# Optimization experiments

Hardware: AMD Instinct MI355X
Metric: run time of the kernel (lower is better)

The kernel has to match this reference:

```python
import jax, jax.numpy as jnp
import numpy as np

WINDOW, HOP = 20, 10   # SplitSignal_cplx(2, window_size=20, hop_length=10)
EPS = 1e-6             # eigenvalue clip for matrix log
RIDGE = 1e-3           # SPD ridge to keep matrices positive definite


def sparsemax(z):
    # Closed-form sparsemax projection onto the simplex (Martins & Astudillo 2016),
    # mirroring use_sparsemax_as_convex_layer (QP projection onto the simplex).
    zs = jnp.sort(z)[::-1]
    k = jnp.arange(1, z.shape[0] + 1, dtype=z.dtype)
    zc = jnp.cumsum(zs)
    support = 1.0 + k * zs > zc
    kz_i = jnp.sum(support).astype(jnp.int32)
    kz = kz_i.astype(z.dtype)
    tau = (zc[kz_i - 1] - 1.0) / kz
    return jnp.maximum(z - tau, 0.0)


def _sym(S):
    return 0.5 * (S + jnp.swapaxes(S, -1, -2))


def logm(S):
    # batched symmetric matrix log via eigh (LogEig / barycenter log-map)
    w, V = jnp.linalg.eigh(_sym(S))
    lw = jnp.log(jnp.maximum(w, EPS))
    return jnp.einsum('...ij,...j,...kj->...ik', V, lw, V)


def expm(S):
    w, V = jnp.linalg.eigh(_sym(S))
    return jnp.einsum('...ij,...j,...kj->...ik', V, jnp.exp(w), V)


def frame_signal(x):
    # x: [B, 2, T] -> frames [B, 2*n_win, WINDOW]  (SplitSignal)
    B, Cc, T = x.shape
    n_win = (T - WINDOW) // HOP + 1
    idx = jnp.arange(n_win)[:, None] * HOP + jnp.arange(WINDOW)[None, :]
    f = x[:, :, idx]                      # [B, 2, n_win, WINDOW]
    return f.reshape(B, Cc * n_win, WINDOW)


def covpool(f):
    # covariance pooling over frames -> SPD [B, WINDOW, WINDOW]
    N = f.shape[1]
    f = f - f.mean(axis=1, keepdims=True)
    cov = jnp.einsum('bnd,bne->bde', f, f) / (N - 1)
    return cov + RIDGE * jnp.eye(WINDOW, dtype=f.dtype)


def cell(S, W, alpha):
    # One DARTS-style SPD cell: candidate BiMap ops + per-channel weighted
    # Riemannian (log-Euclidean) barycenter  G = expm(sum_k w_k logm(op_k(S))).
    # S: [B, C, d, d];  W: [2, K, d, do] (2 branches -> channel doubling);
    # alpha: [K] architecture logits.
    w = sparsemax(alpha)                               # [K]
    cand = jnp.einsum('mkji,bcjl,mkln->mkbcin', W, S, W)  # [2, K, B, C, do, do]
    do = cand.shape[-1]
    cand = cand + RIDGE * jnp.eye(do, dtype=S.dtype)
    L = logm(cand)                                     # log-map of every candidate
    G = expm(jnp.einsum('k,mkbcij->mbcij', w, L))      # weighted barycenter [2,B,C,do,do]
    B = S.shape[0]
    return jnp.moveaxis(G, 0, 1).reshape(B, -1, do, do)  # channels double: [B, 2C, do, do]


def reference(x, W_stem, W_op0, W_op1, W_op2, alphas, W_cls, b_cls):
    f = frame_signal(x)                                # [B, 798, 20]
    cov = covpool(f)                                   # [B, 20, 20]
    # stem BiMap: W^T S W
    S = jnp.einsum('ji,bjk,kl->bil', W_stem, cov, W_stem)[:, None]  # [B,1,20,20]
    S = S + RIDGE * jnp.eye(WINDOW, dtype=x.dtype)
    S = cell(S, W_op0, alphas[0])                      # [B, 2, 10, 10] (reduce 20->10)
    S = cell(S, W_op1, alphas[1])                      # [B, 4, 10, 10]
    S = cell(S, W_op2, alphas[2])                      # [B, 8, 10, 10]
    out = logm(S).reshape(S.shape[0], -1)              # LogEig + flatten -> [B, 800]
    return out @ W_cls + b_cls


def setup_inputs() -> dict:
    key = jax.random.key(0)
    ks = jax.random.split(key, 8)
    B, T = 2048, 4000
    d_in, d_out, K, n_cls = 20, 10, 6, 10
    x = jax.random.normal(ks[0], (B, 2, T), jnp.float32)
    W_stem = jax.random.normal(ks[1], (d_in, d_in), jnp.float32) / np.sqrt(d_in)
    W_op0 = jax.random.normal(ks[2], (2, K, d_in, d_out), jnp.float32) / np.sqrt(d_in)
    W_op1 = jax.random.normal(ks[3], (2, K, d_out, d_out), jnp.float32) / np.sqrt(d_out)
    W_op2 = jax.random.normal(ks[4], (2, K, d_out, d_out), jnp.float32) / np.sqrt(d_out)
    alphas = 0.001 * jax.random.normal(ks[5], (3, K), jnp.float32)
    W_cls = jax.random.normal(ks[6], (8 * d_out * d_out, n_cls), jnp.float32) * 0.02
    b_cls = jnp.zeros((n_cls,), jnp.float32)
    return dict(x=x, W_stem=W_stem, W_op0=W_op0, W_op1=W_op1, W_op2=W_op2,
                alphas=alphas, W_cls=W_cls, b_cls=b_cls)
```

## Files before the change

kernel.cpp:

```cpp
#include <hip/hip_runtime.h>
#include <math.h>

#define WIN   20
#define NWIN  399
#define NCH   2
#define TLEN  4000
#define NFR   798
#define KOPS  6
#define NB    2048
#define EPSV  1e-6f
#define RIDGE 1e-3f

#define TIX(i,j) ((i)*10 - (i)*((i)+1)/2 + (j))

__device__ __forceinline__ float frcp(float x){float r;asm("v_rcp_f32 %0, %1":"=v"(r):"v"(x));return r;}
__device__ __forceinline__ float frsq(float x){float r;asm("v_rsq_f32 %0, %1":"=v"(r):"v"(x));return r;}
__device__ __forceinline__ float fsqr(float x){float r;asm("v_sqrt_f32 %0, %1":"=v"(r):"v"(x));return r;}

__device__ __forceinline__ void jacobi10(float* A, float* V) {
#pragma unroll
  for (int i = 0; i < 100; i++) V[i] = 0.f;
#pragma unroll
  for (int i = 0; i < 10; i++) V[i * 11] = 1.f;

  for (int sweep = 0; sweep < 7; ++sweep) {
    float off = 0.f, dia = 0.f;
#pragma unroll
    for (int p = 0; p < 10; p++) {
      float d = A[TIX(p, p)];
      dia = fmaf(d, d, dia);
#pragma unroll
      for (int q = p + 1; q < 10; q++) { float o = A[TIX(p, q)]; off = fmaf(o, o, off); }
    }
    float fro2 = dia + 2.f * off;
    if (__ballot(off > 1e-11f * fro2) == 0ull) break;
    float skipthr = 1e-12f * fro2;

#pragma unroll
    for (int p = 0; p < 10; p++) {
#pragma unroll
      for (int q = p + 1; q < 10; q++) {
        float apq = A[TIX(p, q)];
        if (__ballot(apq * apq > skipthr) == 0ull) continue;
        float app = A[TIX(p, p)];
        float aqq = A[TIX(q, q)];
        bool rot = fabsf(apq) > 1e-30f;
        float theta = (aqq - app) * frcp(rot ? 2.f * apq : 1.f);
        float t = copysignf(frcp(fabsf(theta) + fsqr(fmaf(theta, theta, 1.f))), theta);
        t = rot ? t : 0.f;
        float c = frsq(fmaf(t, t, 1.f));
        float s = t * c;
#pragma unroll
        for (int j = 0; j < 10; j++) {
          if (j == p || j == q) continue;
          const int jp = (j < p) ? TIX(j, p) : TIX(p, j);
          const int jq = (j < q) ? TIX(j, q) : TIX(q, j);
          float ajp = A[jp], ajq = A[jq];
          A[jp] = fmaf(c, ajp, -s * ajq);
          A[jq] = fmaf(s, ajp, c * ajq);
        }
        A[TIX(p, p)] = fmaf(-t, apq, A[TIX(p, p)]);
        A[TIX(q, q)] = fmaf(t, apq, A[TIX(q, q)]);
        A[TIX(p, q)] = 0.0f;
#pragma unroll
        for (int i = 0; i < 10; i++) {
          float vip = V[i * 10 + p], viq = V[i * 10 + q];
          V[i * 10 + p] = fmaf(c, vip, -s * viq);
          V[i * 10 + q] = fmaf(s, vip, c * viq);
        }
      }
    }
  }
}

__global__ __launch_bounds__(256) void k_cov_stem(const float* __restrict__ x,
                                                  const float* __restrict__ Wst,
                                                  float* __restrict__ Sout) {
  __shared__ float xl[NCH * TLEN];
  __shared__ float pT[2][NCH][100];
  __shared__ float pQ[2][NCH][100];
  __shared__ float bsum[NCH][10];
  __shared__ float b0v[NCH][10];
  __shared__ float b399v[NCH][10];
  __shared__ float cov[400];
  __shared__ float wst[400];
  __shared__ float tmp[400];
  int b = blockIdx.x, tid = threadIdx.x;
  const float4* xg = (const float4*)(x + (size_t)b * NCH * TLEN);
  float4* xl4 = (float4*)xl;
  for (int i = tid; i < NCH * TLEN / 4; i += 256) xl4[i] = xg[i];
  for (int i = tid; i < 400; i += 256) wst[i] = Wst[i];
  __syncthreads();

  if (tid < 200) {
    int grp = tid / 100;
    int c = (tid % 100) / 50;
    int r = tid % 50;
    int seg = r / 25, tile = r % 25;
    int d0 = (tile / 5) * 2, e0 = (tile % 5) * 2;
    const float* xc = xl + c * TLEN;
    int i0 = seg * 200;
    int i1 = grp ? ((seg == 1) ? 399 : 200) : (i0 + 200);
    int eoff = grp ? 10 : 0;
    float a00 = 0.f, a01 = 0.f, a10 = 0.f, a11 = 0.f;
    for (int i = i0; i < i1; i++) {
      float2 bd = *(const float2*)(xc + i * 10 + d0);
      float2 be = *(const float2*)(xc + i * 10 + eoff + e0);
      a00 = fmaf(bd.x, be.x, a00); a01 = fmaf(bd.x, be.y, a01);
      a10 = fmaf(bd.y, be.x, a10); a11 = fmaf(bd.y, be.y, a11);
    }
    float* dst = grp ? &pQ[seg][c][0] : &pT[seg][c][0];
    dst[d0 * 10 + e0] = a00;
    dst[d0 * 10 + e0 + 1] = a01;
    dst[(d0 + 1) * 10 + e0] = a10;
    dst[(d0 + 1) * 10 + e0 + 1] = a11;
  } else if (tid >= 200 && tid < 220) {
    int c = (tid - 200) / 10, d = (tid - 200) % 10;
    const float* xc = xl + c * TLEN;
    float s = 0.f;
    for (int i = 0; i < 400; i++) s += xc[i * 10 + d];
    bsum[c][d] = s;
    b0v[c][d] = xc[d];
    b399v[c][d] = xc[3990 + d];
  }
  __syncthreads();

  const float invN = 1.0f / (float)NFR;
  const float invN1 = 1.0f / (float)(NFR - 1);
  for (int o = tid; o < 400; o += 256) {
    int d = o / 20, e = o % 20;
    int dl = d % 10, el = e % 10;
    float s2;
    if (d < 10 && e < 10)
      s2 = (pT[0][0][dl * 10 + el] + pT[1][0][dl * 10 + el] - b399v[0][dl] * b399v[0][el]) +
           (pT[0][1][dl * 10 + el] + pT[1][1][dl * 10 + el] - b399v[1][dl] * b399v[1][el]);
    else if (d >= 10 && e >= 10)
      s2 = (pT[0][0][dl * 10 + el] + pT[1][0][dl * 10 + el] - b0v[0][dl] * b0v[0][el]) +
           (pT[0][1][dl * 10 + el] + pT[1][1][dl * 10 + el] - b0v[1][dl] * b0v[1][el]);
    else if (d < 10)
      s2 = pQ[0][0][dl * 10 + el] + pQ[1][0][dl * 10 + el] +
           pQ[0][1][dl * 10 + el] + pQ[1][1][dl * 10 + el];
    else
      s2 = pQ[0][0][el * 10 + dl] + pQ[1][0][el * 10 + dl] +
           pQ[0][1][el * 10 + dl] + pQ[1][1][el * 10 + dl];
    float md = (d < 10) ? (bsum[0][dl] - b399v[0][dl] + bsum[1][dl] - b399v[1][dl])
                        : (bsum[0][dl] - b0v[0][dl] + bsum[1][dl] - b0v[1][dl]);
    float me = (e < 10) ? (bsum[0][el] - b399v[0][el] + bsum[1][el] - b399v[1][el])
                        : (bsum[0][el] - b0v[0][el] + bsum[1][el] - b0v[1][el]);
    float v = (s2 - (float)NFR * (md * invN) * (me * invN)) * invN1;
    if (d == e) v += RIDGE;
    cov[o] = v;
  }
  __syncthreads();
  for (int o = tid; o < 400; o += 256) {
    int j = o / 20, l = o % 20;
    float acc = 0.f;
    for (int k2 = 0; k2 < 20; k2++) acc = fmaf(cov[j * 20 + k2], wst[k2 * 20 + l], acc);
    tmp[o] = acc;
  }
  __syncthreads();
  for (int o = tid; o < 400; o += 256) {
    int i = o / 20, l = o % 20;
    float acc = 0.f;
    for (int j = 0; j < 20; j++) acc = fmaf(wst[j * 20 + i], tmp[j * 20 + l], acc);
    if (i == l) acc += RIDGE;
    Sout[b * 400 + o] = acc;
  }
}

__global__ __launch_bounds__(256) void k_cand20(const float* __restrict__ Sin,
                                                const float* __restrict__ Wop,
                                                float* __restrict__ cand, int BC) {
  const int DIN = 20;
  __shared__ float Sl[DIN * DIN];
  __shared__ float Wl[12 * DIN * 10];
  __shared__ float Tl[12 * DIN * 10];
  int bc = blockIdx.x, tid = threadIdx.x;
  for (int i = tid; i < DIN * DIN; i += 256) Sl[i] = Sin[bc * DIN * DIN + i];
  for (int i = tid; i < 12 * DIN * 10; i += 256) Wl[i] = Wop[i];
  __syncthreads();
  for (int o = tid; o < 12 * DIN * 10; o += 256) {
    int mk = o / (DIN * 10);
    int r = o % (DIN * 10);
    int j = r / 10, n = r % 10;
    float acc = 0.f;
    for (int l = 0; l < DIN; l++) acc = fmaf(Sl[j * DIN + l], Wl[mk * DIN * 10 + l * 10 + n], acc);
    Tl[o] = acc;
  }
  __syncthreads();
  int NM = 12 * BC;
  for (int o = tid; o < 12 * 55; o += 256) {
    int mk = o / 55, t = o % 55;
    int t0 = t, i = 0;
    while (t0 >= 10 - i) { t0 -= 10 - i; i++; }
    int n = i + t0;
    float acc = 0.f;
    for (int j = 0; j < DIN; j++)
      acc = fmaf(Wl[mk * DIN * 10 + j * 10 + i], Tl[mk * DIN * 10 + j * 10 + n], acc);
    if (i == n) acc += RIDGE;
    cand[t * NM + mk * BC + bc] = acc;
  }
}

__device__ __forceinline__ void logm_epilogue(float* A, float* V,
                                              float* __restrict__ cand, int NM, int mat) {
  float f[10];
#pragma unroll
  for (int r = 0; r < 10; r++) f[r] = __logf(fmaxf(A[TIX(r, r)], EPSV));
#pragma unroll
  for (int i = 0; i < 10; i++) {
    float w[10];
#pragma unroll
    for (int r = 0; r < 10; r++) w[r] = V[i * 10 + r] * f[r];
#pragma unroll
    for (int n = i; n < 10; n++) {
      float acc = 0.f;
#pragma unroll
      for (int r = 0; r < 10; r++) acc = fmaf(w[r], V[n * 10 + r], acc);
      cand[TIX(i, n) * NM + mat] = acc;
    }
  }
}

__global__ __launch_bounds__(256) void k_logm(float* __restrict__ cand, int NM) {
  int mat = blockIdx.x * 256 + threadIdx.x;
  float A[55];
#pragma unroll
  for (int t = 0; t < 55; t++) A[t] = cand[t * NM + mat];
  float V[100];
  jacobi10(A, V);
  logm_epilogue(A, V, cand, NM, mat);
}

template <int BC>
__global__ __launch_bounds__(256) void k_candlogm(const float* __restrict__ Sin,
                                                  const float* __restrict__ Wop,
                                                  float* __restrict__ cand) {
  __shared__ float Wl[1200];
  int tid = threadIdx.x;
  for (int i = tid; i < 1200; i += 256) Wl[i] = Wop[i];
  __syncthreads();
  const int NM = 12 * BC;
  int mat = blockIdx.x * 256 + tid;
  int mk = mat / BC, bc = mat % BC;
  const float* Wm = Wl + mk * 100;
  const float* Sb = Sin + bc;

  float U[100];
#pragma unroll
  for (int i = 0; i < 100; i++) U[i] = 0.f;
#pragma unroll
  for (int j = 0; j < 10; j++) {
    float sr[10];
#pragma unroll
    for (int l = 0; l < 10; l++) sr[l] = Sb[(j * 10 + l) * BC];
    float wr[10];
#pragma unroll
    for (int i = 0; i < 10; i++) wr[i] = Wm[j * 10 + i];
#pragma unroll
    for (int i = 0; i < 10; i++)
#pragma unroll
      for (int l = 0; l < 10; l++) U[i * 10 + l] = fmaf(wr[i], sr[l], U[i * 10 + l]);
  }
  float A[55];
#pragma unroll
  for (int t = 0; t < 55; t++) A[t] = 0.f;
#pragma unroll
  for (int i = 0; i < 10; i++) A[TIX(i, i)] = RIDGE;
#pragma unroll
  for (int l = 0; l < 10; l++) {
    float wr[10];
#pragma unroll
    for (int n = 0; n < 10; n++) wr[n] = Wm[l * 10 + n];
#pragma unroll
    for (int i = 0; i < 10; i++) {
      float u = U[i * 10 + l];
#pragma unroll
      for (int n = i; n < 10; n++) A[TIX(i, n)] = fmaf(u, wr[n], A[TIX(i, n)]);
    }
  }
  float V[100];
  jacobi10(A, V);
  logm_epilogue(A, V, cand, NM, mat);
}

__device__ __forceinline__ void sparsemax6(const float* __restrict__ a, int row, float* w) {
  float z[KOPS], zs[KOPS];
#pragma unroll
  for (int i = 0; i < KOPS; i++) { z[i] = a[row * KOPS + i]; zs[i] = z[i]; }
#pragma unroll
  for (int i = 0; i < KOPS; i++)
#pragma unroll
    for (int j = i + 1; j < KOPS; j++)
      if (zs[j] > zs[i]) { float tm = zs[i]; zs[i] = zs[j]; zs[j] = tm; }
  float acc = 0.f, zcp = 1.f; float cnt = 1.f;
#pragma unroll
  for (int i = 0; i < KOPS; i++) {
    acc += zs[i];
    if (1.0f + (float)(i + 1) * zs[i] > acc) { cnt = (float)(i + 1); zcp = acc; }
  }
  float tau = (zcp - 1.0f) / cnt;
#pragma unroll
  for (int i = 0; i < KOPS; i++) w[i] = fmaxf(z[i] - tau, 0.0f);
}

template <int BC, int C>
__global__ __launch_bounds__(64) void k_expm(const float* __restrict__ L,
                                             const float* __restrict__ alphas, int row,
                                             float* __restrict__ Sout) {
  const int NM = 12 * BC;
  const int NE = 2 * BC;
  int id = blockIdx.x * 64 + threadIdx.x;
  int m = id / BC;
  int bc = id % BC;
  float w[KOPS];
  sparsemax6(alphas, row, w);
  float A[55];
#pragma unroll
  for (int t = 0; t < 55; t++) {
    float acc = 0.f;
#pragma unroll
    for (int k2 = 0; k2 < KOPS; k2++) acc = fmaf(w[k2], L[t * NM + (m * KOPS + k2) * BC + bc], acc);
    A[t] = acc;
  }
  float V[100];
  jacobi10(A, V);
  float f[10];
#pragma unroll
  for (int r = 0; r < 10; r++) f[r] = __expf(A[TIX(r, r)]);
  int b = bc / C, c = bc % C;
  int idm = b * 2 * C + m * C + c;
  float* out = Sout + idm;
#pragma unroll
  for (int i = 0; i < 10; i++) {
    float wv[10];
#pragma unroll
    for (int r = 0; r < 10; r++) wv[r] = V[i * 10 + r] * f[r];
#pragma unroll
    for (int n = i; n < 10; n++) {
      float acc = 0.f;
#pragma unroll
      for (int r = 0; r < 10; r++) acc = fmaf(wv[r], V[n * 10 + r], acc);
      out[(i * 10 + n) * NE] = acc;
      if (n != i) out[(n * 10 + i) * NE] = acc;
    }
  }
}

__global__ __launch_bounds__(64) void k_final_direct(const float* __restrict__ L,
                                                     const float* __restrict__ alphas,
                                                     const float* __restrict__ Wc,
                                                     const float* __restrict__ bcv,
                                                     float* __restrict__ out) {
  const int BC = 4 * NB;
  const int NM = 12 * BC;
  int id = blockIdx.x * 64 + threadIdx.x;
  int ch = id & 7;
  int b = id >> 3;
  int m = ch >> 2, j = ch & 3;
  int bc = b * 4 + j;
  float w[KOPS];
  sparsemax6(alphas, 2, w);
  const float* Lb = L + (size_t)(m * KOPS) * BC + bc;
  float Z[55];
#pragma unroll
  for (int t = 0; t < 55; t++) {
    float acc = 0.f;
#pragma unroll
    for (int k2 = 0; k2 < KOPS; k2++) acc = fmaf(w[k2], Lb[(size_t)t * NM + k2 * BC], acc);
    Z[t] = acc;
  }
  float acc[10];
#pragma unroll
  for (int c2 = 0; c2 < 10; c2++) acc[c2] = 0.f;
  const float* wbase = Wc + ch * 1000;
#pragma unroll
  for (int i = 0; i < 10; i++) {
#pragma unroll
    for (int n = 0; n < 10; n++) {
      float lv = (i <= n) ? Z[TIX(i, n)] : Z[TIX(n, i)];
      const float* wrow = wbase + (i * 10 + n) * 10;
#pragma unroll
      for (int h = 0; h < 5; h++) {
        float2 wc2 = *(const float2*)(wrow + 2 * h);
        acc[2 * h]     = fmaf(lv, wc2.x, acc[2 * h]);
        acc[2 * h + 1] = fmaf(lv, wc2.y, acc[2 * h + 1]);
      }
    }
  }
#pragma unroll
  for (int mk = 1; mk < 8; mk <<= 1) {
#pragma unroll
    for (int c2 = 0; c2 < 10; c2++) acc[c2] += __shfl_xor(acc[c2], mk, 8);
  }
  if (ch == 0) {
#pragma unroll
    for (int c2 = 0; c2 < 10; c2++) out[b * 10 + c2] = acc[c2] + bcv[c2];
  }
}

extern "C" void kernel_launch(void* const* d_in, const int* in_sizes, int n_in,
                              void* d_out, int out_size, void* d_ws, size_t ws_size,
                              hipStream_t stream) {
  const float* x      = (const float*)d_in[0];
  const float* Wst    = (const float*)d_in[1];
  const float* Wop0   = (const float*)d_in[2];
  const float* Wop1   = (const float*)d_in[3];
  const float* Wop2   = (const float*)d_in[4];
  const float* alphas = (const float*)d_in[5];
  const float* Wcls   = (const float*)d_in[6];
  const float* bcls   = (const float*)d_in[7];
  float* out = (float*)d_out;

  float* ws   = (float*)d_ws;
  float* Sa   = ws;
  float* Sb   = Sa + (size_t)NB * 800;
  float* cand = Sb + (size_t)NB * 800;

  k_cov_stem<<<NB, 256, 0, stream>>>(x, Wst, Sa);

  k_cand20<<<NB, 256, 0, stream>>>(Sa, Wop0, cand, NB);
  k_logm<<<(12 * NB) / 256, 256, 0, stream>>>(cand, 12 * NB);
  k_expm<NB, 1><<<(2 * NB) / 64, 64, 0, stream>>>(cand, alphas, 0, Sb);

  k_candlogm<NB * 2><<<(12 * NB * 2) / 256, 256, 0, stream>>>(Sb, Wop1, cand);
  k_expm<NB * 2, 2><<<(4 * NB) / 64, 64, 0, stream>>>(cand, alphas, 1, Sa);

  k_candlogm<NB * 4><<<(12 * NB * 4) / 256, 256, 0, stream>>>(Sa, Wop2, cand);

  k_final_direct<<<(8 * NB) / 64, 64, 0, stream>>>(cand, alphas, Wcls, bcls, out);
}
```

Measured before the change: 408.7 us.

## Fuse first-cell candidate BiMap into logm kernel and shrink blocks to one wavefront

Replaces the separate k_cand20 and k_logm kernels for the 20->10 cell with one per-thread kernel. Each thread computes its 10x10 candidate from the 20x20 SPD matrix and then runs Jacobi plus the log epilogue, which removes a round trip of candidates through global memory. The stem output is now written in a transposed, batch-minor layout so these loads coalesce. The candlogm kernels move to 64-thread blocks that load only the one weight matrix they need into shared memory. The cost is heavier per-thread register use and redundant 20x20 loads per candidate.

New measurement: 420.9 us. 3.0% more time.

```diff
diff --git a/kernel.cpp b/kernel.cpp
--- a/kernel.cpp
+++ b/kernel.cpp
@@ -164,41 +164,7 @@
     float acc = 0.f;
     for (int j = 0; j < 20; j++) acc = fmaf(wst[j * 20 + i], tmp[j * 20 + l], acc);
     if (i == l) acc += RIDGE;
-    Sout[b * 400 + o] = acc;
-  }
-}
-
-__global__ __launch_bounds__(256) void k_cand20(const float* __restrict__ Sin,
-                                                const float* __restrict__ Wop,
-                                                float* __restrict__ cand, int BC) {
-  const int DIN = 20;
-  __shared__ float Sl[DIN * DIN];
-  __shared__ float Wl[12 * DIN * 10];
-  __shared__ float Tl[12 * DIN * 10];
-  int bc = blockIdx.x, tid = threadIdx.x;
-  for (int i = tid; i < DIN * DIN; i += 256) Sl[i] = Sin[bc * DIN * DIN + i];
-  for (int i = tid; i < 12 * DIN * 10; i += 256) Wl[i] = Wop[i];
-  __syncthreads();
-  for (int o = tid; o < 12 * DIN * 10; o += 256) {
-    int mk = o / (DIN * 10);
-    int r = o % (DIN * 10);
-    int j = r / 10, n = r % 10;
-    float acc = 0.f;
-    for (int l = 0; l < DIN; l++) acc = fmaf(Sl[j * DIN + l], Wl[mk * DIN * 10 + l * 10 + n], acc);
-    Tl[o] = acc;
-  }
-  __syncthreads();
-  int NM = 12 * BC;
-  for (int o = tid; o < 12 * 55; o += 256) {
-    int mk = o / 55, t = o % 55;
-    int t0 = t, i = 0;
-    while (t0 >= 10 - i) { t0 -= 10 - i; i++; }
-    int n = i + t0;
-    float acc = 0.f;
-    for (int j = 0; j < DIN; j++)
-      acc = fmaf(Wl[mk * DIN * 10 + j * 10 + i], Tl[mk * DIN * 10 + j * 10 + n], acc);
-    if (i == n) acc += RIDGE;
-    cand[t * NM + mk * BC + bc] = acc;
+    Sout[o * NB + b] = acc;
   }
 }
 
@@ -222,28 +188,62 @@
   }
 }
 
-__global__ __launch_bounds__(256) void k_logm(float* __restrict__ cand, int NM) {
-  int mat = blockIdx.x * 256 + threadIdx.x;
+__global__ __launch_bounds__(64) void k_candlogm20(const float* __restrict__ Sin,
+                                                   const float* __restrict__ Wop,
+                                                   float* __restrict__ cand) {
+  const int BC = NB;
+  const int NM = 12 * BC;
+  __shared__ float Wl[200];
+  int tid = threadIdx.x;
+  int mat = blockIdx.x * 64 + tid;
+  int mk0 = (blockIdx.x * 64) / BC;
+  for (int i = tid; i < 200; i += 64) Wl[i] = Wop[mk0 * 200 + i];
+  __syncthreads();
+  int bc = mat % BC;
+  const float* Sb = Sin + bc;
+
   float A[55];
 #pragma unroll
-  for (int t = 0; t < 55; t++) A[t] = cand[t * NM + mat];
+  for (int t = 0; t < 55; t++) A[t] = 0.f;
+#pragma unroll
+  for (int i = 0; i < 10; i++) A[TIX(i, i)] = RIDGE;
+#pragma unroll
+  for (int j = 0; j < 20; j++) {
+    float sr[20];
+#pragma unroll
+    for (int l = 0; l < 20; l++) sr[l] = Sb[(j * 20 + l) * BC];
+    float v[10];
+#pragma unroll
+    for (int n = 0; n < 10; n++) {
+      float acc = 0.f;
+#pragma unroll
+      for (int l = 0; l < 20; l++) acc = fmaf(sr[l], Wl[l * 10 + n], acc);
+      v[n] = acc;
+    }
+#pragma unroll
+    for (int i = 0; i < 10; i++) {
+      float wji = Wl[j * 10 + i];
+#pragma unroll
+      for (int n = i; n < 10; n++) A[TIX(i, n)] = fmaf(wji, v[n], A[TIX(i, n)]);
+    }
+  }
   float V[100];
   jacobi10(A, V);
   logm_epilogue(A, V, cand, NM, mat);
 }
 
 template <int BC>
-__global__ __launch_bounds__(256) void k_candlogm(const float* __restrict__ Sin,
-                                                  const float* __restrict__ Wop,
-                                                  float* __restrict__ cand) {
-  __shared__ float Wl[1200];
+__global__ __launch_bounds__(64) void k_candlogm(const float* __restrict__ Sin,
+                                                 const float* __restrict__ Wop,
+                                                 float* __restrict__ cand) {
+  __shared__ float Wl[100];
   int tid = threadIdx.x;
-  for (int i = tid; i < 1200; i += 256) Wl[i] = Wop[i];
-  __syncthreads();
   const int NM = 12 * BC;
-  int mat = blockIdx.x * 256 + tid;
-  int mk = mat / BC, bc = mat % BC;
-  const float* Wm = Wl + mk * 100;
+  int mat = blockIdx.x * 64 + tid;
+  int mk0 = (blockIdx.x * 64) / BC;
+  for (int i = tid; i < 100; i += 64) Wl[i] = Wop[mk0 * 100 + i];
+  __syncthreads();
+  int bc = mat % BC;
   const float* Sb = Sin + bc;
 
   float U[100];
@@ -256,7 +256,7 @@
     for (int l = 0; l < 10; l++) sr[l] = Sb[(j * 10 + l) * BC];
     float wr[10];
 #pragma unroll
-    for (int i = 0; i < 10; i++) wr[i] = Wm[j * 10 + i];
+    for (int i = 0; i < 10; i++) wr[i] = Wl[j * 10 + i];
 #pragma unroll
     for (int i = 0; i < 10; i++)
 #pragma unroll
@@ -271,7 +271,7 @@
   for (int l = 0; l < 10; l++) {
     float wr[10];
 #pragma unroll
-    for (int n = 0; n < 10; n++) wr[n] = Wm[l * 10 + n];
+    for (int n = 0; n < 10; n++) wr[n] = Wl[l * 10 + n];
 #pragma unroll
     for (int i = 0; i < 10; i++) {
       float u = U[i * 10 + l];
@@ -419,14 +419,13 @@
 
   k_cov_stem<<<NB, 256, 0, stream>>>(x, Wst, Sa);
 
-  k_cand20<<<NB, 256, 0, stream>>>(Sa, Wop0, cand, NB);
-  k_logm<<<(12 * NB) / 256, 256, 0, stream>>>(cand, 12 * NB);
+  k_candlogm20<<<(12 * NB) / 64, 64, 0, stream>>>(Sa, Wop0, cand);
   k_expm<NB, 1><<<(2 * NB) / 64, 64, 0, stream>>>(cand, alphas, 0, Sb);
 
-  k_candlogm<NB * 2><<<(12 * NB * 2) / 256, 256, 0, stream>>>(Sb, Wop1, cand);
+  k_candlogm<NB * 2><<<(12 * NB * 2) / 64, 64, 0, stream>>>(Sb, Wop1, cand);
   k_expm<NB * 2, 2><<<(4 * NB) / 64, 64, 0, stream>>>(cand, alphas, 1, Sa);
 
-  k_candlogm<NB * 4><<<(12 * NB * 4) / 256, 256, 0, stream>>>(Sa, Wop2, cand);
+  k_candlogm<NB * 4><<<(12 * NB * 4) / 64, 64, 0, stream>>>(Sa, Wop2, cand);
 
   k_final_direct<<<(8 * NB) / 64, 64, 0, stream>>>(cand, alphas, Wcls, bcls, out);
 }
```
